# Kernel tuning notes

Hardware: AMD Instinct MI355X
Metric: run time of the kernel (lower is better)

Reference implementation:

```python
import jax, jax.numpy as jnp
import numpy as np

# Static config (mirrors cfg.MODEL.LOSSES.Center.*)
ALPHA = 0.5
BETA = 0.1
MARGIN = 50.0
SCALE = 1.0
HARD_MINING = False
B, D, C = 512, 512, 100000


def setup_inputs() -> dict:
    key = jax.random.key(0)
    k1, k2, k3 = jax.random.split(key, 3)
    features = jax.random.normal(k1, (B, D), dtype=jnp.float32)
    labels = jax.random.randint(k2, (B,), 0, C, dtype=jnp.int32)
    centers = jax.random.normal(k3, (C, D), dtype=jnp.float32)
    return {"features": features, "labels": labels, "centers": centers}


def softmax_weights(dist, mask):
    # dist: (B, B) (negative distances), mask: (B, B) in {0, 1}
    min_v = jnp.min(dist * mask, axis=1, keepdims=True)
    numerator = jnp.exp(dist - min_v) * mask  # mask also zeroes out masked entries
    Z = jnp.sum(numerator, axis=1, keepdims=True) + 1e-6
    return numerator / Z


def reference(features, labels, centers):
    labels = labels.astype(jnp.int32)
    # gather, detached (torch: self.centers[labels].detach())
    cg = jax.lax.stop_gradient(centers[labels])  # (B, D)
    delta1 = cg - features  # (B, D)

    center_diff = cg[:, None, :] - cg[None, :, :]  # (B, B, D)
    mask = (labels[None, :] != labels[:, None]).astype(jnp.float32)  # (B, B)
    center_dist = jnp.sqrt(jnp.sum(jnp.square(center_diff), axis=2))  # (B, B)
    mask = mask * (center_dist <= MARGIN).astype(jnp.float32)

    W = softmax_weights(-center_dist, mask)  # (B, B)
    delta2 = jnp.sum(center_diff * W[:, :, None], axis=1)  # (B, D)
    # torch: if mask.sum() < 1: delta2 = zeros
    delta2 = jnp.where(jnp.sum(mask) < 1.0, jnp.zeros_like(delta2), delta2)

    new_vals = cg - ALPHA * delta1 - BETA * delta2  # (B, D)
    new_centers = centers.at[labels].set(jax.lax.stop_gradient(new_vals))

    dist = jnp.clip(jnp.square(cg - features), 1e-12, 1e12)
    loss = jnp.mean(dist) * SCALE
    return loss, new_centers
```

## Files before the change

kernel.cpp:

```cpp
#include <hip/hip_runtime.h>

#define B 512
#define D 512
#define NC 100000
#define BETA 0.1f
#define MARGIN 50.0f
#define TPB 256
#define NFLOAT (NC * D)
#define NG 12800000
#define K0E 2954330
#define K1E 6401047
#define K2E 9355376

typedef float f4 __attribute__((ext_vector_type(4)));

__device__ __forceinline__ void copy_groups(const f4* __restrict__ src4, f4* __restrict__ dst4,
                                            int lo, int hi, int widx, int wstride)
{
    const int lane = widx & 63;
    int g = lo + widx;
    for (; (g - lane) + 63 + 7 * wstride < hi; g += 8 * wstride) {
        f4 v[8];
        #pragma unroll
        for (int u = 0; u < 8; ++u) v[u] = src4[g + u * wstride];
        float pw[8];
        #pragma unroll
        for (int u = 0; u < 8; ++u) {
            pw[u] = __shfl_up(v[u].w, 1, 64);
            if (lane == 0) pw[u] = src4[g + u * wstride - 1].w;
        }
        #pragma unroll
        for (int u = 0; u < 8; ++u) {
            f4 o = { pw[u], v[u].x, v[u].y, v[u].z };
            __builtin_nontemporal_store(o, dst4 + (g + u * wstride));
        }
    }
    for (; (g - lane) < hi; g += wstride) {
        int gc = (g < hi) ? g : (hi - 1);
        f4 v = src4[gc];
        float pw = __shfl_up(v.w, 1, 64);
        if (lane == 0) pw = src4[gc - 1].w;
        if (g < hi) {
            f4 o = { pw, v.x, v.y, v.z };
            __builtin_nontemporal_store(o, dst4 + g);
        }
    }
}

__global__ __launch_bounds__(TPB) void k0_gather(
    const float* __restrict__ centers, const float* __restrict__ features,
    const int* __restrict__ labels, float* __restrict__ cgbuf,
    float* __restrict__ rowLoss, int* __restrict__ winner, float* __restrict__ outAll)
{
    const int b = blockIdx.x, t = threadIdx.x;
    if (b < B) {
        __shared__ float red[TPB];
        __shared__ int labs[B];
        __shared__ int wsh;
        labs[t] = labels[t]; labs[t + 256] = labels[t + 256];
        if (t == 0) wsh = 1;
        __syncthreads();
        const int i = b;
        const int li = labs[i];
        const float2* crow = (const float2*)(centers + (size_t)li * D);
        const float2* frow = (const float2*)(features + (size_t)i * D);
        float2 c = crow[t], f = frow[t];
        ((float2*)(cgbuf + (size_t)i * D))[t] = c;
        float dx = c.x - f.x, dy = c.y - f.y;
        red[t] = fminf(fmaxf(dx * dx, 1e-12f), 1e12f) + fminf(fmaxf(dy * dy, 1e-12f), 1e12f);
        for (int j = i + 1 + t; j < B; j += TPB)
            if (labs[j] == li) wsh = 0;
        __syncthreads();
        for (int s = 128; s; s >>= 1) { if (t < s) red[t] += red[t + s]; __syncthreads(); }
        if (t == 0) { rowLoss[i] = red[0]; winner[i] = wsh; }
    } else {
        copy_groups((const f4*)centers, (f4*)outAll, 1, K0E, (b - 512) * TPB + t, 1536 * TPB);
    }
}

__global__ __launch_bounds__(TPB) void k1_pairdist(
    const float* __restrict__ centers, const float* __restrict__ cgbuf,
    float* __restrict__ dist, float* __restrict__ outAll)
{
    const int b = blockIdx.x, t = threadIdx.x;
    if (b < 256) {
        __shared__ float As[16][33];
        __shared__ float Bs[16][33];
        const int bi = b >> 4, bj = b & 15;
        const int tx = t & 15, ty = t >> 4;
        float a00 = 0.f, a01 = 0.f, a10 = 0.f, a11 = 0.f;
        for (int k0 = 0; k0 < D; k0 += 16) {
            #pragma unroll
            for (int it = 0; it < 2; ++it) {
                int idx = t + it * 256;
                int r = idx >> 4, kk = idx & 15;
                As[kk][r] = cgbuf[(size_t)(bi * 32 + r) * D + k0 + kk];
                Bs[kk][r] = cgbuf[(size_t)(bj * 32 + r) * D + k0 + kk];
            }
            __syncthreads();
            #pragma unroll
            for (int kk = 0; kk < 16; ++kk) {
                float x0 = As[kk][ty * 2], x1 = As[kk][ty * 2 + 1];
                float y0 = Bs[kk][tx * 2], y1 = Bs[kk][tx * 2 + 1];
                float d00 = x0 - y0, d01 = x0 - y1, d10 = x1 - y0, d11 = x1 - y1;
                a00 += d00 * d00; a01 += d01 * d01; a10 += d10 * d10; a11 += d11 * d11;
            }
            __syncthreads();
        }
        int r0 = bi * 32 + ty * 2, c0 = bj * 32 + tx * 2;
        dist[r0 * B + c0]           = sqrtf(a00);
        dist[r0 * B + c0 + 1]       = sqrtf(a01);
        dist[(r0 + 1) * B + c0]     = sqrtf(a10);
        dist[(r0 + 1) * B + c0 + 1] = sqrtf(a11);
    } else {
        copy_groups((const f4*)centers, (f4*)outAll, K0E, K1E, (b - 256) * TPB + t, 1792 * TPB);
    }
}

__global__ __launch_bounds__(TPB) void k2_softmax(
    const float* __restrict__ centers, const float* __restrict__ dist,
    const int* __restrict__ labels, float* __restrict__ Wm,
    float* __restrict__ rowS, float* __restrict__ rowCnt, float* __restrict__ outAll)
{
    const int b = blockIdx.x, t = threadIdx.x;
    if (b < B) {
        __shared__ float red[TPB];
        __shared__ int labs[B];
        labs[t] = labels[t]; labs[t + 256] = labels[t + 256];
        __syncthreads();
        const int i = b;
        const int li = labs[i];
        float d0 = dist[i * B + t], d1 = dist[i * B + t + 256];
        int m0 = (labs[t] != li) && (d0 <= MARGIN);
        int m1 = (labs[t + 256] != li) && (d1 <= MARGIN);
        red[t] = fmaxf(m0 ? d0 : 0.f, m1 ? d1 : 0.f); __syncthreads();
        for (int s = 128; s; s >>= 1) { if (t < s) red[t] = fmaxf(red[t], red[t + s]); __syncthreads(); }
        float maxd = red[0]; __syncthreads();
        float n0 = m0 ? expf(maxd - d0) : 0.f;
        float n1 = m1 ? expf(maxd - d1) : 0.f;
        red[t] = n0 + n1; __syncthreads();
        for (int s = 128; s; s >>= 1) { if (t < s) red[t] += red[t + s]; __syncthreads(); }
        float Z = red[0] + 1e-6f; __syncthreads();
        float invZ = 1.f / Z;
        Wm[i * B + t]       = n0 * invZ;
        Wm[i * B + t + 256] = n1 * invZ;
        red[t] = (float)(m0 + m1); __syncthreads();
        for (int s = 128; s; s >>= 1) { if (t < s) red[t] += red[t + s]; __syncthreads(); }
        if (t == 0) { rowS[i] = (Z - 1e-6f) * invZ; rowCnt[i] = red[0]; }
    } else {
        copy_groups((const f4*)centers, (f4*)outAll, K1E, K2E, (b - 512) * TPB + t, 1536 * TPB);
    }
}

__global__ __launch_bounds__(TPB) void k3_gemm(
    const float* __restrict__ features, const float* __restrict__ centers,
    const float* __restrict__ cgbuf, const float* __restrict__ Wm,
    const float* __restrict__ rowS, const float* __restrict__ rowCnt,
    const float* __restrict__ rowLoss, float* __restrict__ vals,
    float* __restrict__ out, float* __restrict__ outAll)
{
    const int b = blockIdx.x, t = threadIdx.x;
    float* outC = out + 1;
    if (b < 256) {
        __shared__ float red[TPB];
        __shared__ float As[16][33];
        __shared__ float Bs[16][33];
        __shared__ float fsh;
        red[t] = rowCnt[t] + rowCnt[t + 256]; __syncthreads();
        for (int s = 128; s; s >>= 1) { if (t < s) red[t] += red[t + s]; __syncthreads(); }
        if (t == 0) fsh = (red[0] < 1.0f) ? 0.f : 1.f;
        __syncthreads();
        const float flagv = fsh;
        const int bi = b >> 4, bj = b & 15;
        const int tx = t & 15, ty = t >> 4;
        float a00 = 0.f, a01 = 0.f, a10 = 0.f, a11 = 0.f;
        for (int j0 = 0; j0 < B; j0 += 16) {
            #pragma unroll
            for (int it = 0; it < 2; ++it) {
                int idx = t + it * 256;
                int r = idx >> 4, jj = idx & 15;
                As[jj][r] = Wm[(size_t)(bi * 32 + r) * B + j0 + jj];
                int c = idx & 31, jj2 = idx >> 5;
                Bs[jj2][c] = cgbuf[(size_t)(j0 + jj2) * D + bj * 32 + c];
            }
            __syncthreads();
            #pragma unroll
            for (int kk = 0; kk < 16; ++kk) {
                float w0 = As[kk][ty * 2], w1 = As[kk][ty * 2 + 1];
                float c0 = Bs[kk][tx * 2], c1 = Bs[kk][tx * 2 + 1];
                a00 += w0 * c0; a01 += w0 * c1; a10 += w1 * c0; a11 += w1 * c1;
            }
            __syncthreads();
        }
        const int i0 = bi * 32 + ty * 2, i1 = i0 + 1;
        const int dcol = bj * 32 + tx * 2;
        float s0 = rowS[i0], s1 = rowS[i1];
        float c, f;
        c = cgbuf[(size_t)i0 * D + dcol];     f = features[(size_t)i0 * D + dcol];
        vals[(size_t)i0 * D + dcol]     = 0.5f * (c + f) - BETA * flagv * (s0 * c - a00);
        c = cgbuf[(size_t)i0 * D + dcol + 1]; f = features[(size_t)i0 * D + dcol + 1];
        vals[(size_t)i0 * D + dcol + 1] = 0.5f * (c + f) - BETA * flagv * (s0 * c - a01);
        c = cgbuf[(size_t)i1 * D + dcol];     f = features[(size_t)i1 * D + dcol];
        vals[(size_t)i1 * D + dcol]     = 0.5f * (c + f) - BETA * flagv * (s1 * c - a10);
        c = cgbuf[(size_t)i1 * D + dcol + 1]; f = features[(size_t)i1 * D + dcol + 1];
        vals[(size_t)i1 * D + dcol + 1] = 0.5f * (c + f) - BETA * flagv * (s1 * c - a11);
    } else if (b == 256) {
        __shared__ float red[TPB];
        red[t] = rowLoss[t] + rowLoss[t + 256]; __syncthreads();
        for (int s = 128; s; s >>= 1) { if (t < s) red[t] += red[t + s]; __syncthreads(); }
        if (t == 0) out[0] = red[0] * (1.0f / ((float)B * (float)D));
        if (t == 1) { outC[0] = centers[0]; outC[1] = centers[1]; outC[2] = centers[2]; }
        if (t == 2) { outC[NFLOAT - 1] = centers[NFLOAT - 1]; }
    } else {
        copy_groups((const f4*)centers, (f4*)outAll, K2E, NG, (b - 257) * TPB + t, 1791 * TPB);
    }
}

__global__ __launch_bounds__(TPB) void k4_scatter(
    const float* __restrict__ vals, const int* __restrict__ labels,
    const int* __restrict__ winner, float* __restrict__ outC)
{
    const int b = blockIdx.x, t = threadIdx.x;
    const int i = b * 2 + (t >> 7);
    const int dcol = (t & 127) * 4;
    if (!winner[i]) return;
    f4 v;
    __builtin_memcpy(&v, &vals[(size_t)i * D + dcol], 16);
    float* dst = outC + (size_t)labels[i] * D + dcol;
    __builtin_memcpy(dst, &v, 16);
}

extern "C" void kernel_launch(void* const* d_in, const int* in_sizes, int n_in,
                              void* d_out, int out_size, void* d_ws, size_t ws_size,
                              hipStream_t stream)
{
    const float* features = (const float*)d_in[0];
    const int*   labels   = (const int*)d_in[1];
    const float* centers  = (const float*)d_in[2];

    float* out  = (float*)d_out;
    float* outC = out + 1;

    char* ws = (char*)d_ws;
    float* cgbuf   = (float*)(ws);
    float* dist    = (float*)(ws + 1048576);
    float* Wm      = (float*)(ws + 2097152);
    float* vals    = (float*)(ws + 3145728);
    float* rowLoss = (float*)(ws + 4194304);
    float* rowS    = (float*)(ws + 4196352);
    float* rowCnt  = (float*)(ws + 4198400);
    int*   winner  = (int*)  (ws + 4200448);

    k0_gather<<<2048, TPB, 0, stream>>>(centers, features, labels, cgbuf, rowLoss, winner, out);
    k1_pairdist<<<2048, TPB, 0, stream>>>(centers, cgbuf, dist, out);
    k2_softmax<<<2048, TPB, 0, stream>>>(centers, dist, labels, Wm, rowS, rowCnt, out);
    k3_gemm<<<2048, TPB, 0, stream>>>(features, centers, cgbuf, Wm, rowS, rowCnt,
                                      rowLoss, vals, out, out);
    k4_scatter<<<256, TPB, 0, stream>>>(vals, labels, winner, outC);
}
```

Baseline: 101.8 us.

## Fuse softmax stage into GEMM kernel and split center copy across three kernels

Removes the separate softmax kernel. Each GEMM block now recomputes row max and normalizer from the distance matrix and builds the softmax weights on the fly while loading tiles. The global mask-count flag is accumulated atomically in the pairdist kernel. The background centers copy changes from a grid-strided layout to contiguous per-block spans spread over three kernels instead of four. This cuts one launch and the W-matrix round trip, at the cost of redundant exp/softmax work repeated across the 16 column blocks.

```diff
diff --git a/kernel.cpp b/kernel.cpp
--- a/kernel.cpp
+++ b/kernel.cpp
@@ -8,55 +8,63 @@
 #define TPB 256
 #define NFLOAT (NC * D)
 #define NG 12800000
-#define K0E 2954330
-#define K1E 6401047
-#define K2E 9355376
+#define KAE 4350001
+#define KBE 8700001
 
 typedef float f4 __attribute__((ext_vector_type(4)));
 
-__device__ __forceinline__ void copy_groups(const f4* __restrict__ src4, f4* __restrict__ dst4,
-                                            int lo, int hi, int widx, int wstride)
-{
-    const int lane = widx & 63;
-    int g = lo + widx;
-    for (; (g - lane) + 63 + 7 * wstride < hi; g += 8 * wstride) {
+__device__ __forceinline__ void copy_span(const f4* __restrict__ src4, f4* __restrict__ dst4,
+                                          int lo, int hi, int bi, int nblk, int tid)
+{
+    const int total = hi - lo;
+    const int per = (total + nblk - 1) / nblk;
+    const int s = lo + bi * per;
+    int e = s + per; if (e > hi) e = hi;
+    if (s >= hi) return;
+    const int lane = tid & 63;
+    int base = s;
+    for (; base + 8 * TPB <= e; base += 8 * TPB) {
+        const int g = base + tid;
         f4 v[8];
         #pragma unroll
-        for (int u = 0; u < 8; ++u) v[u] = src4[g + u * wstride];
+        for (int u = 0; u < 8; ++u) v[u] = src4[g + u * TPB];
         float pw[8];
         #pragma unroll
         for (int u = 0; u < 8; ++u) {
             pw[u] = __shfl_up(v[u].w, 1, 64);
-            if (lane == 0) pw[u] = src4[g + u * wstride - 1].w;
+            if (lane == 0) pw[u] = src4[g + u * TPB - 1].w;
         }
         #pragma unroll
         for (int u = 0; u < 8; ++u) {
             f4 o = { pw[u], v[u].x, v[u].y, v[u].z };
-            __builtin_nontemporal_store(o, dst4 + (g + u * wstride));
-        }
-    }
-    for (; (g - lane) < hi; g += wstride) {
-        int gc = (g < hi) ? g : (hi - 1);
+            __builtin_nontemporal_store(o, dst4 + (g + u * TPB));
+        }
+    }
+    for (; base < e; base += TPB) {
+        const int g = base + tid;
+        const int gc = (g < hi) ? g : (hi - 1);
         f4 v = src4[gc];
         float pw = __shfl_up(v.w, 1, 64);
         if (lane == 0) pw = src4[gc - 1].w;
-        if (g < hi) {
+        if (g < e) {
             f4 o = { pw, v.x, v.y, v.z };
             __builtin_nontemporal_store(o, dst4 + g);
         }
     }
 }
 
-__global__ __launch_bounds__(TPB) void k0_gather(
+__global__ __launch_bounds__(TPB) void kA_gather(
     const float* __restrict__ centers, const float* __restrict__ features,
     const int* __restrict__ labels, float* __restrict__ cgbuf,
-    float* __restrict__ rowLoss, int* __restrict__ winner, float* __restrict__ outAll)
+    float* __restrict__ rowLoss, int* __restrict__ winner, int* __restrict__ maskCnt,
+    float* __restrict__ outAll)
 {
     const int b = blockIdx.x, t = threadIdx.x;
     if (b < B) {
         __shared__ float red[TPB];
         __shared__ int labs[B];
         __shared__ int wsh;
+        if (b == 0 && t == 0) *maskCnt = 0;
         labs[t] = labels[t]; labs[t + 256] = labels[t + 256];
         if (t == 0) wsh = 1;
         __syncthreads();
@@ -74,18 +82,20 @@
         for (int s = 128; s; s >>= 1) { if (t < s) red[t] += red[t + s]; __syncthreads(); }
         if (t == 0) { rowLoss[i] = red[0]; winner[i] = wsh; }
     } else {
-        copy_groups((const f4*)centers, (f4*)outAll, 1, K0E, (b - 512) * TPB + t, 1536 * TPB);
-    }
-}
-
-__global__ __launch_bounds__(TPB) void k1_pairdist(
-    const float* __restrict__ centers, const float* __restrict__ cgbuf,
-    float* __restrict__ dist, float* __restrict__ outAll)
+        copy_span((const f4*)centers, (f4*)outAll, 1, KAE, b - 512, 1536, t);
+    }
+}
+
+__global__ __launch_bounds__(TPB) void kB_pairdist(
+    const float* __restrict__ centers, const int* __restrict__ labels,
+    const float* __restrict__ cgbuf, float* __restrict__ dist,
+    int* __restrict__ maskCnt, float* __restrict__ outAll)
 {
     const int b = blockIdx.x, t = threadIdx.x;
     if (b < 256) {
         __shared__ float As[16][33];
         __shared__ float Bs[16][33];
+        __shared__ int redI[TPB];
         const int bi = b >> 4, bj = b & 15;
         const int tx = t & 15, ty = t >> 4;
         float a00 = 0.f, a01 = 0.f, a10 = 0.f, a11 = 0.f;
@@ -107,71 +117,74 @@
             }
             __syncthreads();
         }
-        int r0 = bi * 32 + ty * 2, c0 = bj * 32 + tx * 2;
-        dist[r0 * B + c0]           = sqrtf(a00);
-        dist[r0 * B + c0 + 1]       = sqrtf(a01);
-        dist[(r0 + 1) * B + c0]     = sqrtf(a10);
-        dist[(r0 + 1) * B + c0 + 1] = sqrtf(a11);
+        const int r0 = bi * 32 + ty * 2, c0 = bj * 32 + tx * 2;
+        float s00 = sqrtf(a00), s01 = sqrtf(a01), s10 = sqrtf(a10), s11 = sqrtf(a11);
+        dist[r0 * B + c0]           = s00;
+        dist[r0 * B + c0 + 1]       = s01;
+        dist[(r0 + 1) * B + c0]     = s10;
+        dist[(r0 + 1) * B + c0 + 1] = s11;
+        const int lr0 = labels[r0], lr1 = labels[r0 + 1];
+        const int lc0 = labels[c0], lc1 = labels[c0 + 1];
+        int cnt = 0;
+        cnt += (lr0 != lc0) && (s00 <= MARGIN);
+        cnt += (lr0 != lc1) && (s01 <= MARGIN);
+        cnt += (lr1 != lc0) && (s10 <= MARGIN);
+        cnt += (lr1 != lc1) && (s11 <= MARGIN);
+        redI[t] = cnt; __syncthreads();
+        for (int s = 128; s; s >>= 1) { if (t < s) redI[t] += redI[t + s]; __syncthreads(); }
+        if (t == 0 && redI[0] > 0) atomicAdd(maskCnt, redI[0]);
     } else {
-        copy_groups((const f4*)centers, (f4*)outAll, K0E, K1E, (b - 256) * TPB + t, 1792 * TPB);
-    }
-}
-
-__global__ __launch_bounds__(TPB) void k2_softmax(
-    const float* __restrict__ centers, const float* __restrict__ dist,
-    const int* __restrict__ labels, float* __restrict__ Wm,
-    float* __restrict__ rowS, float* __restrict__ rowCnt, float* __restrict__ outAll)
-{
-    const int b = blockIdx.x, t = threadIdx.x;
-    if (b < B) {
-        __shared__ float red[TPB];
-        __shared__ int labs[B];
-        labs[t] = labels[t]; labs[t + 256] = labels[t + 256];
-        __syncthreads();
-        const int i = b;
-        const int li = labs[i];
-        float d0 = dist[i * B + t], d1 = dist[i * B + t + 256];
-        int m0 = (labs[t] != li) && (d0 <= MARGIN);
-        int m1 = (labs[t + 256] != li) && (d1 <= MARGIN);
-        red[t] = fmaxf(m0 ? d0 : 0.f, m1 ? d1 : 0.f); __syncthreads();
-        for (int s = 128; s; s >>= 1) { if (t < s) red[t] = fmaxf(red[t], red[t + s]); __syncthreads(); }
-        float maxd = red[0]; __syncthreads();
-        float n0 = m0 ? expf(maxd - d0) : 0.f;
-        float n1 = m1 ? expf(maxd - d1) : 0.f;
-        red[t] = n0 + n1; __syncthreads();
-        for (int s = 128; s; s >>= 1) { if (t < s) red[t] += red[t + s]; __syncthreads(); }
-        float Z = red[0] + 1e-6f; __syncthreads();
-        float invZ = 1.f / Z;
-        Wm[i * B + t]       = n0 * invZ;
-        Wm[i * B + t + 256] = n1 * invZ;
-        red[t] = (float)(m0 + m1); __syncthreads();
-        for (int s = 128; s; s >>= 1) { if (t < s) red[t] += red[t + s]; __syncthreads(); }
-        if (t == 0) { rowS[i] = (Z - 1e-6f) * invZ; rowCnt[i] = red[0]; }
-    } else {
-        copy_groups((const f4*)centers, (f4*)outAll, K1E, K2E, (b - 512) * TPB + t, 1536 * TPB);
-    }
-}
-
-__global__ __launch_bounds__(TPB) void k3_gemm(
-    const float* __restrict__ features, const float* __restrict__ centers,
-    const float* __restrict__ cgbuf, const float* __restrict__ Wm,
-    const float* __restrict__ rowS, const float* __restrict__ rowCnt,
+        copy_span((const f4*)centers, (f4*)outAll, KAE, KBE, b - 256, 1792, t);
+    }
+}
+
+__global__ __launch_bounds__(TPB) void kC_gemm(
+    const float* __restrict__ features, const int* __restrict__ labels,
+    const float* __restrict__ centers, const float* __restrict__ cgbuf,
+    const float* __restrict__ dist, const int* __restrict__ maskCnt,
     const float* __restrict__ rowLoss, float* __restrict__ vals,
     float* __restrict__ out, float* __restrict__ outAll)
 {
     const int b = blockIdx.x, t = threadIdx.x;
     float* outC = out + 1;
     if (b < 256) {
-        __shared__ float red[TPB];
         __shared__ float As[16][33];
         __shared__ float Bs[16][33];
-        __shared__ float fsh;
-        red[t] = rowCnt[t] + rowCnt[t + 256]; __syncthreads();
-        for (int s = 128; s; s >>= 1) { if (t < s) red[t] += red[t + s]; __syncthreads(); }
-        if (t == 0) fsh = (red[0] < 1.0f) ? 0.f : 1.f;
-        __syncthreads();
-        const float flagv = fsh;
+        __shared__ int labs[B];
+        __shared__ float mxs[32], invZs[32], rowSsh[32];
+        labs[t] = labels[t]; labs[t + 256] = labels[t + 256];
+        __syncthreads();
         const int bi = b >> 4, bj = b & 15;
+        {
+            const int rg = t >> 3, lg = t & 7;
+            const int row = bi * 32 + rg;
+            const int lr = labs[row];
+            const float* drow = dist + row * B;
+            float mx = 0.f;
+            for (int k = 0; k < 64; ++k) {
+                int j = lg + 8 * k;
+                float d = drow[j];
+                bool m = (labs[j] != lr) && (d <= MARGIN);
+                mx = fmaxf(mx, m ? d : 0.f);
+            }
+            #pragma unroll
+            for (int o = 1; o < 8; o <<= 1) mx = fmaxf(mx, __shfl_xor(mx, o, 64));
+            float sum = 0.f;
+            for (int k = 0; k < 64; ++k) {
+                int j = lg + 8 * k;
+                float d = drow[j];
+                bool m = (labs[j] != lr) && (d <= MARGIN);
+                sum += m ? expf(mx - d) : 0.f;
+            }
+            #pragma unroll
+            for (int o = 1; o < 8; o <<= 1) sum += __shfl_xor(sum, o, 64);
+            if (lg == 0) {
+                float Z = sum + 1e-6f;
+                mxs[rg] = mx; invZs[rg] = 1.f / Z; rowSsh[rg] = sum / Z;
+            }
+        }
+        __syncthreads();
+        const float flagv = (*maskCnt > 0) ? 1.f : 0.f;
         const int tx = t & 15, ty = t >> 4;
         float a00 = 0.f, a01 = 0.f, a10 = 0.f, a11 = 0.f;
         for (int j0 = 0; j0 < B; j0 += 16) {
@@ -179,7 +192,10 @@
             for (int it = 0; it < 2; ++it) {
                 int idx = t + it * 256;
                 int r = idx >> 4, jj = idx & 15;
-                As[jj][r] = Wm[(size_t)(bi * 32 + r) * B + j0 + jj];
+                int j = j0 + jj;
+                float d = dist[(size_t)(bi * 32 + r) * B + j];
+                bool m = (labs[j] != labs[bi * 32 + r]) && (d <= MARGIN);
+                As[jj][r] = m ? expf(mxs[r] - d) * invZs[r] : 0.f;
                 int c = idx & 31, jj2 = idx >> 5;
                 Bs[jj2][c] = cgbuf[(size_t)(j0 + jj2) * D + bj * 32 + c];
             }
@@ -194,7 +210,7 @@
         }
         const int i0 = bi * 32 + ty * 2, i1 = i0 + 1;
         const int dcol = bj * 32 + tx * 2;
-        float s0 = rowS[i0], s1 = rowS[i1];
+        const float s0 = rowSsh[ty * 2], s1 = rowSsh[ty * 2 + 1];
         float c, f;
         c = cgbuf[(size_t)i0 * D + dcol];     f = features[(size_t)i0 * D + dcol];
         vals[(size_t)i0 * D + dcol]     = 0.5f * (c + f) - BETA * flagv * (s0 * c - a00);
@@ -212,11 +228,11 @@
         if (t == 1) { outC[0] = centers[0]; outC[1] = centers[1]; outC[2] = centers[2]; }
         if (t == 2) { outC[NFLOAT - 1] = centers[NFLOAT - 1]; }
     } else {
-        copy_groups((const f4*)centers, (f4*)outAll, K2E, NG, (b - 257) * TPB + t, 1791 * TPB);
-    }
-}
-
-__global__ __launch_bounds__(TPB) void k4_scatter(
+        copy_span((const f4*)centers, (f4*)outAll, KBE, NG, b - 257, 1791, t);
+    }
+}
+
+__global__ __launch_bounds__(TPB) void kD_scatter(
     const float* __restrict__ vals, const int* __restrict__ labels,
     const int* __restrict__ winner, float* __restrict__ outC)
 {
@@ -244,17 +260,15 @@
     char* ws = (char*)d_ws;
     float* cgbuf   = (float*)(ws);
     float* dist    = (float*)(ws + 1048576);
-    float* Wm      = (float*)(ws + 2097152);
-    float* vals    = (float*)(ws + 3145728);
-    float* rowLoss = (float*)(ws + 4194304);
-    float* rowS    = (float*)(ws + 4196352);
-    float* rowCnt  = (float*)(ws + 4198400);
-    int*   winner  = (int*)  (ws + 4200448);
-
-    k0_gather<<<2048, TPB, 0, stream>>>(centers, features, labels, cgbuf, rowLoss, winner, out);
-    k1_pairdist<<<2048, TPB, 0, stream>>>(centers, cgbuf, dist, out);
-    k2_softmax<<<2048, TPB, 0, stream>>>(centers, dist, labels, Wm, rowS, rowCnt, out);
-    k3_gemm<<<2048, TPB, 0, stream>>>(features, centers, cgbuf, Wm, rowS, rowCnt,
+    float* vals    = (float*)(ws + 2097152);
+    float* rowLoss = (float*)(ws + 3145728);
+    int*   winner  = (int*)  (ws + 3147776);
+    int*   maskCnt = (int*)  (ws + 3149824);
+
+    kA_gather<<<2048, TPB, 0, stream>>>(centers, features, labels, cgbuf, rowLoss,
+                                        winner, maskCnt, out);
+    kB_pairdist<<<2048, TPB, 0, stream>>>(centers, labels, cgbuf, dist, maskCnt, out);
+    kC_gemm<<<2048, TPB, 0, stream>>>(features, labels, centers, cgbuf, dist, maskCnt,
                                       rowLoss, vals, out, out);
-    k4_scatter<<<256, TPB, 0, stream>>>(vals, labels, winner, outC);
-}
+    kD_scatter<<<256, TPB, 0, stream>>>(vals, labels, winner, outC);
+}
```

Result: slower. 124.2 us (+22.0%).
